# Kernel optimization log

Measured on AMD Instinct MI355X. Metric: run time of the kernel, lower is better.

The kernel has to match this reference:

```python
import jax, jax.numpy as jnp
import numpy as np

N_NODES = 100000
N_PART = 5000
N_EDGES = 1000000
D_NODE = 128
D_PART = 128
D_ATT = 20


def setup_inputs() -> dict:
    key = jax.random.key(0)
    ks = jax.random.split(key, 20)
    inp = {
        "nodes_hidden": jax.random.normal(ks[0], (N_NODES, D_NODE), jnp.float32),
        "particles_hidden": jax.random.normal(ks[1], (N_PART, D_PART), jnp.float32),
        "global_rep": jax.random.normal(ks[2], (N_PART, D_NODE), jnp.float32),
        "src": jax.random.randint(ks[3], (N_EDGES,), 0, N_NODES, jnp.int32),
        "dst": jax.random.randint(ks[4], (N_EDGES,), 0, N_PART, jnp.int32),
        "key_W": jax.random.normal(ks[5], (D_NODE, D_ATT), jnp.float32) * 0.05,
        "key_b": jnp.zeros((D_ATT,), jnp.float32),
        "val_W": jax.random.normal(ks[6], (D_NODE, D_PART), jnp.float32) * 0.05,
        "val_b": jnp.zeros((D_PART,), jnp.float32),
        "q_W": jax.random.normal(ks[7], (D_PART + D_NODE, D_ATT), jnp.float32) * 0.05,
        "q_b": jnp.zeros((D_ATT,), jnp.float32),
        "W_ih": jax.random.normal(ks[8], (3 * D_PART, D_PART), jnp.float32) * 0.05,
        "W_hh": jax.random.normal(ks[9], (3 * D_PART, D_PART), jnp.float32) * 0.05,
        "b_ih": jnp.zeros((3 * D_PART,), jnp.float32),
        "b_hh": jnp.zeros((3 * D_PART,), jnp.float32),
        "ln_g": jnp.ones((D_PART,), jnp.float32),
        "ln_b": jnp.zeros((D_PART,), jnp.float32),
        "mlp_W1": jax.random.normal(ks[10], (D_PART, 64), jnp.float32) * 0.05,
        "mlp_b1": jnp.zeros((64,), jnp.float32),
        "mlp_W2": jax.random.normal(ks[11], (64, D_PART), jnp.float32) * 0.05,
        "mlp_b2": jnp.zeros((D_PART,), jnp.float32),
    }
    return inp


def reference(nodes_hidden, particles_hidden, global_rep, src, dst,
              key_W, key_b, val_W, val_b, q_W, q_b,
              W_ih, W_hh, b_ih, b_hh, ln_g, ln_b,
              mlp_W1, mlp_b1, mlp_W2, mlp_b2):
    norm = jnp.float32(1.0) / jnp.sqrt(jnp.float32(D_ATT))
    keys = nodes_hidden @ key_W + key_b          # [N, 20]
    vals = nodes_hidden @ val_W + val_b          # [N, P]
    q_in = jnp.concatenate([particles_hidden, global_rep], axis=1)
    query = q_in @ q_W + q_b                     # [Np, 20]

    # per-edge raw attention (ReLU'd copy in edges.data is unused downstream)
    att = jnp.sum(keys[src] * query[dst], axis=1) * norm     # [E]
    msg = att[:, None] * vals[src]                            # [E, P]
    weighted_sum = jax.ops.segment_sum(msg, dst, num_segments=particles_hidden.shape[0])

    # GRUCell(input=weighted_sum, hidden=particles_hidden), torch semantics
    gi = weighted_sum @ W_ih.T + b_ih
    gh = particles_hidden @ W_hh.T + b_hh
    i_r, i_z, i_n = jnp.split(gi, 3, axis=1)
    h_r, h_z, h_n = jnp.split(gh, 3, axis=1)
    r = jax.nn.sigmoid(i_r + h_r)
    z = jax.nn.sigmoid(i_z + h_z)
    n = jnp.tanh(i_n + r * h_n)
    h_new = (1.0 - z) * n + z * particles_hidden

    # LayerNorm (eps=1e-5)
    mu = jnp.mean(h_new, axis=-1, keepdims=True)
    var = jnp.mean(jnp.square(h_new - mu), axis=-1, keepdims=True)
    ln = (h_new - mu) * jax.lax.rsqrt(var + 1e-5) * ln_g + ln_b

    mlp_out = jax.nn.relu(ln @ mlp_W1 + mlp_b1) @ mlp_W2 + mlp_b2
    return particles_hidden + mlp_out
```

## Files before the change

### kernel.cpp

```cpp
#include <hip/hip_runtime.h>
#include <math.h>

#define N_NODES 100000
#define N_PART  5000
#define N_EDGES 1000000
#define D_NODE  128
#define D_PART  128
#define D_ATT   20
#define NBLK    128
#define EPB     ((N_EDGES + NBLK - 1) / NBLK)
#define TPV6    8
#define QBLKS   (N_PART / TPV6)

__device__ __forceinline__ float sigmoid_(float x) { return 1.f / (1.f + __expf(-x)); }
__device__ __forceinline__ float tanh_(float x)    { return 1.f - 2.f / (__expf(2.f * x) + 1.f); }

__device__ __forceinline__ void gru_body(float4 acc[4],
    float4 w0, float4 w1, float4 w2, float4 w3,
    float4 x0, float4 x1, float4 x2, float4 x3)
{
    acc[0].x += x0.x * w0.x + x0.y * w1.x + x0.z * w2.x + x0.w * w3.x;
    acc[0].y += x0.x * w0.y + x0.y * w1.y + x0.z * w2.y + x0.w * w3.y;
    acc[0].z += x0.x * w0.z + x0.y * w1.z + x0.z * w2.z + x0.w * w3.z;
    acc[0].w += x0.x * w0.w + x0.y * w1.w + x0.z * w2.w + x0.w * w3.w;
    acc[1].x += x1.x * w0.x + x1.y * w1.x + x1.z * w2.x + x1.w * w3.x;
    acc[1].y += x1.x * w0.y + x1.y * w1.y + x1.z * w2.y + x1.w * w3.y;
    acc[1].z += x1.x * w0.z + x1.y * w1.z + x1.z * w2.z + x1.w * w3.z;
    acc[1].w += x1.x * w0.w + x1.y * w1.w + x1.z * w2.w + x1.w * w3.w;
    acc[2].x += x2.x * w0.x + x2.y * w1.x + x2.z * w2.x + x2.w * w3.x;
    acc[2].y += x2.x * w0.y + x2.y * w1.y + x2.z * w2.y + x2.w * w3.y;
    acc[2].z += x2.x * w0.z + x2.y * w1.z + x2.z * w2.z + x2.w * w3.z;
    acc[2].w += x2.x * w0.w + x2.y * w1.w + x2.z * w2.w + x2.w * w3.w;
    acc[3].x += x3.x * w0.x + x3.y * w1.x + x3.z * w2.x + x3.w * w3.x;
    acc[3].y += x3.x * w0.y + x3.y * w1.y + x3.z * w2.y + x3.w * w3.y;
    acc[3].z += x3.x * w0.z + x3.y * w1.z + x3.z * w2.z + x3.w * w3.z;
    acc[3].w += x3.x * w0.w + x3.y * w1.w + x3.z * w2.w + x3.w * w3.w;
}

__global__ __launch_bounds__(256) void fused_front_kernel(
    const float* __restrict__ valW, const float* __restrict__ Wih,
    const float* __restrict__ Whh, float* __restrict__ Wbig,
    const float* __restrict__ valb, float* __restrict__ bvec,
    const int* __restrict__ dst, int* __restrict__ totals,
    const float* __restrict__ ph, const float* __restrict__ gr,
    const float* __restrict__ qW, const float* __restrict__ qb,
    const float* __restrict__ keyW, const float* __restrict__ keyb,
    float* __restrict__ qk, float* __restrict__ qoff)
{
    __shared__ float pool[5000];
    int blk = blockIdx.x;
    int t = threadIdx.x;

    if (blk < 12) {
        float (*sA)[33] = (float (*)[33])pool;
        float (*sB)[33] = (float (*)[33])(pool + 2112);
        int bk = blk / 6, bj = blk - bk * 6;
        int k0 = bk * 64, j0 = bj * 64;
        int tk = t >> 4, tj = t & 15;
        float acc[4][4];
        #pragma unroll
        for (int i = 0; i < 4; i++)
            #pragma unroll
            for (int j = 0; j < 4; j++) acc[i][j] = 0.f;

        for (int mc = 0; mc < 128; mc += 32) {
            #pragma unroll
            for (int s = 0; s < 2; s++) {
                int f = t + s * 256;
                int r = f >> 3, c4 = (f & 7) * 4;
                *(float4*)&sA[r][c4] = *(const float4*)(valW + (size_t)(k0 + r) * 128 + mc + c4);
                *(float4*)&sB[r][c4] = *(const float4*)(Wih  + (size_t)(j0 + r) * 128 + mc + c4);
            }
            __syncthreads();
            #pragma unroll 8
            for (int mm = 0; mm < 32; mm++) {
                float a0 = sA[tk * 4 + 0][mm], a1 = sA[tk * 4 + 1][mm];
                float a2 = sA[tk * 4 + 2][mm], a3 = sA[tk * 4 + 3][mm];
                float b0 = sB[tj * 4 + 0][mm], b1 = sB[tj * 4 + 1][mm];
                float b2 = sB[tj * 4 + 2][mm], b3 = sB[tj * 4 + 3][mm];
                acc[0][0] += a0 * b0; acc[0][1] += a0 * b1; acc[0][2] += a0 * b2; acc[0][3] += a0 * b3;
                acc[1][0] += a1 * b0; acc[1][1] += a1 * b1; acc[1][2] += a1 * b2; acc[1][3] += a1 * b3;
                acc[2][0] += a2 * b0; acc[2][1] += a2 * b1; acc[2][2] += a2 * b2; acc[2][3] += a2 * b3;
                acc[3][0] += a3 * b0; acc[3][1] += a3 * b1; acc[3][2] += a3 * b2; acc[3][3] += a3 * b3;
            }
            __syncthreads();
        }
        #pragma unroll
        for (int i = 0; i < 4; i++) {
            int k = k0 + tk * 4 + i;
            #pragma unroll
            for (int j = 0; j < 4; j++) {
                int oj = j0 + tj * 4 + j;
                Wbig[(size_t)k * 512 + (oj & 127) * 4 + (oj >> 7)] = acc[i][j];
            }
        }
    } else if (blk < 14) {
        for (int f = t; f < 8192; f += 256) {
            int e = (blk - 12) * 8192 + f;
            int k = e >> 7, c = e & 127;
            Wbig[(size_t)k * 512 + c * 4 + 3] = 0.f;
        }
    } else if (blk < 142) {
        #pragma unroll
        for (int s = 0; s < 2; s++) {
            int idx = 65536 + (blk - 14) * 512 + s * 256 + t;
            int k = idx >> 9;
            int jn = idx & 511;
            int j = (jn & 3) * 128 + (jn >> 2);
            int kp = k - 128;
            float v = 0.f;
            if (j < 256)       v = Whh[j * 128 + kp];
            else if (j >= 384) v = Whh[(j - 128) * 128 + kp];
            Wbig[(size_t)k * 512 + jn] = v;
        }
    } else if (blk < 144) {
        int c = (blk - 142) * 256 + t;
        if (c < 384) {
            float acc = 0.f;
            #pragma unroll 8
            for (int m = 0; m < 128; m++) acc += valb[m] * Wih[c * 128 + m];
            bvec[c] = acc;
        }
    } else if (blk < 272) {
        int b = blk - 144;
        int* h = (int*)pool;
        for (int i = t; i < N_PART; i += 256) h[i] = 0;
        __syncthreads();
        int beg = b * EPB, end = min(beg + EPB, N_EDGES);
        for (int e = beg + t; e < end; e += 256)
            atomicAdd(&h[dst[e]], 1);
        __syncthreads();
        for (int i = t; i < N_PART; i += 256)
            if (h[i]) atomicAdd(&totals[i], h[i]);
    } else {
        float (*s_in)[260] = (float (*)[260])pool;
        float (*s_q)[20]   = (float (*)[20])(pool + 2080);
        float (*s_kw)[21]  = (float (*)[21])(pool + 2240);
        float* s_kb = pool + 4928;
        float* s_qb = pool + 4948;

        int pbase = (blk - 272) * TPV6;

        for (int f = t; f < TPV6 * 64; f += 256) {
            int pl = f >> 6, r = f & 63;
            int c4 = r * 4;
            int p = pbase + pl;
            float4 v;
            if (c4 < 128) v = *(const float4*)(ph + (size_t)p * 128 + c4);
            else          v = *(const float4*)(gr + (size_t)p * 128 + (c4 - 128));
            *(float4*)&s_in[pl][c4] = v;
        }
        for (int f = t; f < 2560; f += 256) {
            int j = f / 20, a = f - j * 20;
            s_kw[j][a] = keyW[f];
        }
        if (t < 20) { s_kb[t] = keyb[t]; s_qb[t] = qb[t]; }
        __syncthreads();

        if (t < 160) {
            int pl = t / 20, a = t - (t / 20) * 20;
            float acc = s_qb[a];
            const float* qwp = qW + a;
            #pragma unroll 8
            for (int k = 0; k < 256; k++) acc += s_in[pl][k] * qwp[k * 20];
            s_q[pl][a] = acc;
        }
        __syncthreads();

        {
            int pl = t >> 5, j0 = (t & 31) * 4;
            float acc0 = 0.f, acc1 = 0.f, acc2 = 0.f, acc3 = 0.f;
            #pragma unroll
            for (int a = 0; a < 20; a++) {
                float qv = s_q[pl][a];
                acc0 += qv * s_kw[j0][a];
                acc1 += qv * s_kw[j0 + 1][a];
                acc2 += qv * s_kw[j0 + 2][a];
                acc3 += qv * s_kw[j0 + 3][a];
            }
            float4 o; o.x = acc0; o.y = acc1; o.z = acc2; o.w = acc3;
            *(float4*)(qk + (size_t)(pbase + pl) * 128 + j0) = o;

            if (t < TPV6) {
                float acc = 0.f;
                #pragma unroll
                for (int a = 0; a < 20; a++) acc += s_kb[a] * s_q[t][a];
                qoff[pbase + t] = acc;
            }
        }
    }
}

__global__ __launch_bounds__(256) void scan_kernel(
    const int* __restrict__ totals, int* __restrict__ offsets,
    int* __restrict__ cur)
{
    __shared__ int ss[256];
    int t = threadIdx.x;
    const int CH = 20;
    int beg = t * CH;
    int end = min(beg + CH, N_PART);
    int lsum = 0;
    for (int i = beg; i < end; i++) lsum += totals[i];
    ss[t] = lsum;
    __syncthreads();
    for (int off = 1; off < 256; off <<= 1) {
        int v = (t >= off) ? ss[t - off] : 0;
        __syncthreads();
        ss[t] += v;
        __syncthreads();
    }
    int base = ss[t] - lsum;
    for (int i = beg; i < end; i++) {
        offsets[i] = base;
        cur[i] = base;
        base += totals[i];
    }
    if (t == 0) offsets[N_PART] = N_EDGES;
}

__global__ __launch_bounds__(256) void scatter_atomic_kernel(
    const int* __restrict__ src, const int* __restrict__ dst,
    int* __restrict__ cur, int* __restrict__ ssrc)
{
    int stride = gridDim.x * 256;
    for (int e = blockIdx.x * 256 + threadIdx.x; e < N_EDGES; e += stride) {
        int d = dst[e];
        int pos = atomicAdd(&cur[d], 1);
        ssrc[pos] = src[e];
    }
}

__global__ __launch_bounds__(256) void edge_agg_kernel(
    const float* __restrict__ nodes, const float* __restrict__ qk,
    const float* __restrict__ qoff,
    const int* __restrict__ offsets, const int* __restrict__ ssrc,
    float* __restrict__ agg, float* __restrict__ att_sum)
{
    const float norm = 0.22360679774997896f;
    int p = blockIdx.x;
    int tid = threadIdx.x;
    int lane = tid & 63;
    int wave = tid >> 6;
    int half = lane >> 5;
    int colq = (lane & 31) * 4;

    const float4 q = *(const float4*)(qk + (size_t)p * 128 + colq);
    float qo = qoff[p];
    int beg = offsets[p], end = offsets[p + 1];
    int n = end - beg;
    int np = (n + 1) >> 1;
    int npfull = n >> 1;

    float4 a = {0.f, 0.f, 0.f, 0.f};
    float asum = 0.f;

    int pi = wave;
    for (; pi + 12 < npfull; pi += 16) {
        int e0 = beg + 2 * pi + half;
        int s0 = ssrc[e0];
        int s1 = ssrc[e0 + 8];
        int s2 = ssrc[e0 + 16];
        int s3 = ssrc[e0 + 24];
        float4 x0 = *(const float4*)(nodes + (size_t)s0 * 128 + colq);
        float4 x1 = *(const float4*)(nodes + (size_t)s1 * 128 + colq);
        float4 x2 = *(const float4*)(nodes + (size_t)s2 * 128 + colq);
        float4 x3 = *(const float4*)(nodes + (size_t)s3 * 128 + colq);
        float d0 = x0.x * q.x + x0.y * q.y + x0.z * q.z + x0.w * q.w;
        float d1 = x1.x * q.x + x1.y * q.y + x1.z * q.z + x1.w * q.w;
        float d2 = x2.x * q.x + x2.y * q.y + x2.z * q.z + x2.w * q.w;
        float d3 = x3.x * q.x + x3.y * q.y + x3.z * q.z + x3.w * q.w;
        #pragma unroll
        for (int off = 1; off <= 16; off <<= 1) {
            d0 += __shfl_xor(d0, off, 64);
            d1 += __shfl_xor(d1, off, 64);
            d2 += __shfl_xor(d2, off, 64);
            d3 += __shfl_xor(d3, off, 64);
        }
        float t0 = (d0 + qo) * norm;
        float t1 = (d1 + qo) * norm;
        float t2 = (d2 + qo) * norm;
        float t3 = (d3 + qo) * norm;
        a.x += t0 * x0.x + t1 * x1.x + t2 * x2.x + t3 * x3.x;
        a.y += t0 * x0.y + t1 * x1.y + t2 * x2.y + t3 * x3.y;
        a.z += t0 * x0.z + t1 * x1.z + t2 * x2.z + t3 * x3.z;
        a.w += t0 * x0.w + t1 * x1.w + t2 * x2.w + t3 * x3.w;
        asum += t0 + t1 + t2 + t3;
    }
    for (; pi < np; pi += 4) {
        int e0 = beg + 2 * pi;
        bool has1 = (e0 + 1 < end);
        int s0 = ssrc[e0];
        int s1 = has1 ? ssrc[e0 + 1] : s0;
        int s = half ? s1 : s0;
        float4 x = *(const float4*)(nodes + (size_t)s * 128 + colq);
        float d = x.x * q.x + x.y * q.y + x.z * q.z + x.w * q.w;
        #pragma unroll
        for (int off = 1; off <= 16; off <<= 1) d += __shfl_xor(d, off, 64);
        float att = (d + qo) * norm;
        if (half && !has1) att = 0.f;
        a.x += att * x.x; a.y += att * x.y; a.z += att * x.z; a.w += att * x.w;
        asum += att;
    }

    a.x += __shfl_xor(a.x, 32, 64);
    a.y += __shfl_xor(a.y, 32, 64);
    a.z += __shfl_xor(a.z, 32, 64);
    a.w += __shfl_xor(a.w, 32, 64);
    asum += __shfl_xor(asum, 32, 64);

    __shared__ float s_acc[4][128];
    __shared__ float s_as[4];
    if (lane < 32) {
        *(float4*)&s_acc[wave][colq] = a;
        if (lane == 0) s_as[wave] = asum;
    }
    __syncthreads();

    if (tid < 128) {
        float v = s_acc[0][tid] + s_acc[1][tid] + s_acc[2][tid] + s_acc[3][tid];
        agg[(size_t)p * 128 + tid] = v;
        if (tid == 0) att_sum[p] = s_as[0] + s_as[1] + s_as[2] + s_as[3];
    }
}

__global__ __launch_bounds__(256) void gru_fused_v6(
    const float* __restrict__ agg, const float* __restrict__ att_sum,
    const float* __restrict__ ph,
    const float* __restrict__ Wbig, const float* __restrict__ bvec,
    const float* __restrict__ bih, const float* __restrict__ bhh,
    const float* __restrict__ lng, const float* __restrict__ lnb,
    const float* __restrict__ W1, const float* __restrict__ b1,
    const float* __restrict__ W2, const float* __restrict__ b2,
    float* __restrict__ out)
{
    __shared__ float s_in[TPV6][256];
    __shared__ float s_ln[TPV6][128];
    __shared__ float s_hid[TPV6][64];

    int t = threadIdx.x;
    int pbase = blockIdx.x * TPV6;

    for (int f = t; f < TPV6 * 64; f += 256) {
        int pl = f >> 6, r = f & 63;
        int c4 = r * 4;
        int p = pbase + pl;
        float4 v;
        if (c4 < 128) v = *(const float4*)(agg + (size_t)p * 128 + c4);
        else          v = *(const float4*)(ph + (size_t)p * 128 + (c4 - 128));
        *(float4*)&s_in[pl][c4] = v;
    }

    int c  = t & 127;
    int j4 = c * 4;
    int pg = t >> 7;
    float4 cb, bv;
    cb.x = bih[c]       + bhh[c];        bv.x = bvec[c];
    cb.y = bih[128 + c] + bhh[128 + c];  bv.y = bvec[128 + c];
    cb.z = bih[256 + c];                 bv.z = bvec[256 + c];
    cb.w = bhh[256 + c];                 bv.w = 0.f;
    float4 acc[4];
    #pragma unroll
    for (int i = 0; i < 4; i++) {
        float as = att_sum[pbase + pg * 4 + i];
        acc[i].x = cb.x + as * bv.x;
        acc[i].y = cb.y + as * bv.y;
        acc[i].z = cb.z + as * bv.z;
        acc[i].w = cb.w + as * bv.w;
    }
    __syncthreads();

    const float* wp = Wbig + j4;
    float4 w0 = *(const float4*)(wp);
    float4 w1 = *(const float4*)(wp + 512);
    float4 w2 = *(const float4*)(wp + 1024);
    float4 w3 = *(const float4*)(wp + 1536);
    float4 x0 = *(const float4*)&s_in[pg * 4 + 0][0];
    float4 x1 = *(const float4*)&s_in[pg * 4 + 1][0];
    float4 x2 = *(const float4*)&s_in[pg * 4 + 2][0];
    float4 x3 = *(const float4*)&s_in[pg * 4 + 3][0];
    for (int k = 0; k < 256; k += 4) {
        float4 cw0 = w0, cw1 = w1, cw2 = w2, cw3 = w3;
        float4 cx0 = x0, cx1 = x1, cx2 = x2, cx3 = x3;
        if (k < 252) {
            const float* wn = wp + (size_t)(k + 4) * 512;
            w0 = *(const float4*)(wn);
            w1 = *(const float4*)(wn + 512);
            w2 = *(const float4*)(wn + 1024);
            w3 = *(const float4*)(wn + 1536);
            x0 = *(const float4*)&s_in[pg * 4 + 0][k + 4];
            x1 = *(const float4*)&s_in[pg * 4 + 1][k + 4];
            x2 = *(const float4*)&s_in[pg * 4 + 2][k + 4];
            x3 = *(const float4*)&s_in[pg * 4 + 3][k + 4];
        }
        gru_body(acc, cw0, cw1, cw2, cw3, cx0, cx1, cx2, cx3);
    }

    #pragma unroll
    for (int i = 0; i < 4; i++) {
        int pl = pg * 4 + i;
        float r = sigmoid_(acc[i].x);
        float z = sigmoid_(acc[i].y);
        float n = tanh_(acc[i].z + r * acc[i].w);
        float h = s_in[pl][128 + c];
        s_ln[pl][c] = (1.f - z) * n + z * h;
    }
    __syncthreads();

    {
        int wv = t >> 6, l = t & 63;
        for (int pl = wv; pl < TPV6; pl += 4) {
            float v0 = s_ln[pl][l * 2], v1 = s_ln[pl][l * 2 + 1];
            float sum = v0 + v1, sq = v0 * v0 + v1 * v1;
            #pragma unroll
            for (int off = 1; off <= 32; off <<= 1) {
                sum += __shfl_xor(sum, off, 64);
                sq  += __shfl_xor(sq, off, 64);
            }
            float mu = sum * (1.f / 128.f);
            float var = sq * (1.f / 128.f) - mu * mu;
            float rstd = rsqrtf(var + 1e-5f);
            s_ln[pl][l * 2]     = (v0 - mu) * rstd * lng[l * 2] + lnb[l * 2];
            s_ln[pl][l * 2 + 1] = (v1 - mu) * rstd * lng[l * 2 + 1] + lnb[l * 2 + 1];
        }
    }
    __syncthreads();

    for (int idx = t; idx < TPV6 * 64; idx += 256) {
        int pl = idx >> 6, u = idx & 63;
        float a0 = b1[u];
        #pragma unroll 4
        for (int k = 0; k < 128; k++) a0 += s_ln[pl][k] * W1[k * 64 + u];
        s_hid[pl][u] = fmaxf(a0, 0.f);
    }
    __syncthreads();

    for (int idx = t; idx < TPV6 * 32; idx += 256) {
        int pl = idx >> 5, qd = idx & 31;
        int c4 = qd * 4;
        float4 o = *(const float4*)(b2 + c4);
        #pragma unroll 4
        for (int u = 0; u < 64; u++) {
            float av = s_hid[pl][u];
            float4 w = *(const float4*)(W2 + u * 128 + c4);
            o.x += av * w.x; o.y += av * w.y; o.z += av * w.z; o.w += av * w.w;
        }
        float4 h4 = *(const float4*)&s_in[pl][128 + c4];
        float4 res;
        res.x = h4.x + o.x; res.y = h4.y + o.y;
        res.z = h4.z + o.z; res.w = h4.w + o.w;
        *(float4*)(out + (size_t)(pbase + pl) * 128 + c4) = res;
    }
}

extern "C" void kernel_launch(void* const* d_in, const int* in_sizes, int n_in,
                              void* d_out, int out_size, void* d_ws, size_t ws_size,
                              hipStream_t stream) {
    const float* nodes = (const float*)d_in[0];
    const float* ph    = (const float*)d_in[1];
    const float* gr    = (const float*)d_in[2];
    const int*   src   = (const int*)d_in[3];
    const int*   dst   = (const int*)d_in[4];
    const float* keyW  = (const float*)d_in[5];
    const float* keyb  = (const float*)d_in[6];
    const float* valW  = (const float*)d_in[7];
    const float* valb  = (const float*)d_in[8];
    const float* qW    = (const float*)d_in[9];
    const float* qb    = (const float*)d_in[10];
    const float* Wih   = (const float*)d_in[11];
    const float* Whh   = (const float*)d_in[12];
    const float* bih   = (const float*)d_in[13];
    const float* bhh   = (const float*)d_in[14];
    const float* lng   = (const float*)d_in[15];
    const float* lnb   = (const float*)d_in[16];
    const float* W1    = (const float*)d_in[17];
    const float* b1    = (const float*)d_in[18];
    const float* W2    = (const float*)d_in[19];
    const float* b2    = (const float*)d_in[20];
    float* out = (float*)d_out;

    float* ws_f      = (float*)d_ws;
    float* qk        = ws_f;
    float* qoff      = qk + 640000;
    float* agg       = qoff + 5008;
    float* att_sum   = agg + 640000;
    int*   totals    = (int*)(att_sum + 5008);
    int*   offsets   = totals + 5008;
    int*   cur       = offsets + 5008;
    int*   ssrc      = cur + 5008;
    float* Wbig      = (float*)(ssrc + 1000000);
    float* bvec      = Wbig + 131072;

    hipMemsetAsync(totals, 0, N_PART * sizeof(int), stream);

    fused_front_kernel<<<272 + QBLKS, 256, 0, stream>>>(
        valW, Wih, Whh, Wbig,
        valb, bvec,
        dst, totals,
        ph, gr, qW, qb, keyW, keyb, qk, qoff);

    scan_kernel<<<1, 256, 0, stream>>>(totals, offsets, cur);

    scatter_atomic_kernel<<<512, 256, 0, stream>>>(src, dst, cur, ssrc);

    edge_agg_kernel<<<N_PART, 256, 0, stream>>>(nodes, qk, qoff, offsets, ssrc, agg, att_sum);

    gru_fused_v6<<<N_PART / TPV6, 256, 0, stream>>>(
        agg, att_sum, ph, Wbig, bvec, bih, bhh, lng, lnb, W1, b1, W2, b2, out);
}
```

Baseline: 316.1 us.

## Replace global-atomic edge scatter with per-block histogram offsets and LDS atomics

The counting sort of edges by destination now stores a per-block histogram instead of atomically adding into global totals. A new column-scan kernel turns those histograms into per-block exclusive offsets and totals. The scatter kernel then uses shared-memory cursors per block, which replaces global atomics on 5000 hot counters with LDS atomics. The cost is an extra kernel launch, a 128x5000 int buffer written and read twice, and a serial 128-step column scan per particle.

```diff
diff --git a/kernel.cpp b/kernel.cpp
--- a/kernel.cpp
+++ b/kernel.cpp
@@ -41,7 +41,7 @@
     const float* __restrict__ valW, const float* __restrict__ Wih,
     const float* __restrict__ Whh, float* __restrict__ Wbig,
     const float* __restrict__ valb, float* __restrict__ bvec,
-    const int* __restrict__ dst, int* __restrict__ totals,
+    const int* __restrict__ dst, int* __restrict__ blockhist,
     const float* __restrict__ ph, const float* __restrict__ gr,
     const float* __restrict__ qW, const float* __restrict__ qb,
     const float* __restrict__ keyW, const float* __restrict__ keyb,
@@ -131,7 +131,7 @@
             atomicAdd(&h[dst[e]], 1);
         __syncthreads();
         for (int i = t; i < N_PART; i += 256)
-            if (h[i]) atomicAdd(&totals[i], h[i]);
+            blockhist[(size_t)b * N_PART + i] = h[i];
     } else {
         float (*s_in)[260] = (float (*)[260])pool;
         float (*s_q)[20]   = (float (*)[20])(pool + 2080);
@@ -191,9 +191,23 @@
     }
 }
 
+__global__ __launch_bounds__(256) void colscan_kernel(
+    int* __restrict__ blockhist, int* __restrict__ totals)
+{
+    int i = blockIdx.x * 256 + threadIdx.x;
+    if (i >= N_PART) return;
+    int run = 0;
+    for (int b = 0; b < NBLK; b++) {
+        size_t idx = (size_t)b * N_PART + i;
+        int v = blockhist[idx];
+        blockhist[idx] = run;
+        run += v;
+    }
+    totals[i] = run;
+}
+
 __global__ __launch_bounds__(256) void scan_kernel(
-    const int* __restrict__ totals, int* __restrict__ offsets,
-    int* __restrict__ cur)
+    const int* __restrict__ totals, int* __restrict__ offsets)
 {
     __shared__ int ss[256];
     int t = threadIdx.x;
@@ -213,18 +227,23 @@
     int base = ss[t] - lsum;
     for (int i = beg; i < end; i++) {
         offsets[i] = base;
-        cur[i] = base;
         base += totals[i];
     }
     if (t == 0) offsets[N_PART] = N_EDGES;
 }
 
-__global__ __launch_bounds__(256) void scatter_atomic_kernel(
+__global__ __launch_bounds__(256) void scatter_sorted_kernel(
     const int* __restrict__ src, const int* __restrict__ dst,
-    int* __restrict__ cur, int* __restrict__ ssrc)
-{
-    int stride = gridDim.x * 256;
-    for (int e = blockIdx.x * 256 + threadIdx.x; e < N_EDGES; e += stride) {
+    const int* __restrict__ offsets, const int* __restrict__ blockhist,
+    int* __restrict__ ssrc)
+{
+    __shared__ int cur[N_PART];
+    int b = blockIdx.x;
+    for (int i = threadIdx.x; i < N_PART; i += 256)
+        cur[i] = offsets[i] + blockhist[(size_t)b * N_PART + i];
+    __syncthreads();
+    int beg = b * EPB, end = min(beg + EPB, N_EDGES);
+    for (int e = beg + threadIdx.x; e < end; e += 256) {
         int d = dst[e];
         int pos = atomicAdd(&cur[d], 1);
         ssrc[pos] = src[e];
@@ -486,22 +505,22 @@
     float* att_sum   = agg + 640000;
     int*   totals    = (int*)(att_sum + 5008);
     int*   offsets   = totals + 5008;
-    int*   cur       = offsets + 5008;
-    int*   ssrc      = cur + 5008;
+    int*   blockhist = offsets + 5008;
+    int*   ssrc      = blockhist + (size_t)NBLK * N_PART;
     float* Wbig      = (float*)(ssrc + 1000000);
     float* bvec      = Wbig + 131072;
-
-    hipMemsetAsync(totals, 0, N_PART * sizeof(int), stream);
 
     fused_front_kernel<<<272 + QBLKS, 256, 0, stream>>>(
         valW, Wih, Whh, Wbig,
         valb, bvec,
-        dst, totals,
+        dst, blockhist,
         ph, gr, qW, qb, keyW, keyb, qk, qoff);
 
-    scan_kernel<<<1, 256, 0, stream>>>(totals, offsets, cur);
-
-    scatter_atomic_kernel<<<512, 256, 0, stream>>>(src, dst, cur, ssrc);
+    colscan_kernel<<<(N_PART + 255) / 256, 256, 0, stream>>>(blockhist, totals);
+
+    scan_kernel<<<1, 256, 0, stream>>>(totals, offsets);
+
+    scatter_sorted_kernel<<<NBLK, 256, 0, stream>>>(src, dst, offsets, blockhist, ssrc);
 
     edge_agg_kernel<<<N_PART, 256, 0, stream>>>(nodes, qk, qoff, offsets, ssrc, agg, att_sum);
 
```

Result: faster. 283.5 us (-10.3%).
